# Performance work log

Measured on AMD Instinct MI355X. Metric: run time of the kernel, lower is better.

The kernel has to match this reference:

```python
import jax, jax.numpy as jnp
import numpy as np

N_NODES = 100000
N_EDGES = 1280000
IN_DIM = 64
OUT_DIM = 64


def setup_inputs() -> dict:
    key = jax.random.key(0)
    k1, k2, k3, k4, k5 = jax.random.split(key, 5)
    features = jax.random.normal(k1, (N_NODES, IN_DIM), dtype=jnp.float32)
    w = jax.random.uniform(k2, (N_EDGES,), dtype=jnp.float32)
    # torch nn.Linear weight is [out, in]; we store it as [in, out] so h @ W
    W = jax.random.normal(k3, (IN_DIM, OUT_DIM), dtype=jnp.float32) * (1.0 / np.sqrt(IN_DIM))
    src = jax.random.randint(k4, (N_EDGES,), 0, N_NODES, dtype=jnp.int64 if jax.config.jax_enable_x64 else jnp.int32)
    dst = jax.random.randint(k5, (N_EDGES,), 0, N_NODES, dtype=jnp.int64 if jax.config.jax_enable_x64 else jnp.int32)
    return {"features": features, "w": w, "W": W, "src": src, "dst": dst}


def reference(features, w, W, src, dst):
    num_nodes = features.shape[0]
    # u_mul_e: per-edge message = h[src] * w  (edge-weighted SpMM gather-multiply)
    msg = features[src] * w[:, None]                     # [E, in_dim]
    # fn.sum('m','h'): scatter-add messages to destination nodes
    agg = jax.ops.segment_sum(msg, dst, num_segments=num_nodes)  # [N, in_dim]
    # D_in = 1 / clamp(in_degree, min=1)
    deg = jax.ops.segment_sum(jnp.ones_like(w), dst, num_segments=num_nodes)
    d_in = 1.0 / jnp.maximum(deg, 1.0)                   # [N]
    h = agg * d_in[:, None]
    # linear (bias=False), activation None, batch_norm False, dropout 0
    return h @ W                                         # [N, out_dim]
```

## Files before the change

### kernel.cpp

```cpp
#include <hip/hip_runtime.h>

#define N_NODES 100000
#define N_EDGES 1280000
#define DIM 64
#define NBINS 391
#define CAP 3712
#define EPB 4096
#define NFB 313
#define CONVB 512
#define NTILES 1563
#define FPAD 68
#define WSCALE (1.0f / 32767.0f)

__device__ __forceinline__ unsigned bf16_rne(float x) {
    unsigned u = __float_as_uint(x);
    return (u + 0x7fffu + ((u >> 16) & 1u)) >> 16;
}
__device__ __forceinline__ float bf_lo(unsigned q) { return __uint_as_float(q << 16); }
__device__ __forceinline__ float bf_hi(unsigned q) { return __uint_as_float(q & 0xffff0000u); }

__global__ __launch_bounds__(256) void k_fill_conv(
    const int* __restrict__ src, const float* __restrict__ w,
    const int* __restrict__ dst, int* __restrict__ cursor,
    uint2* __restrict__ binned,
    const float* __restrict__ feat, const float* __restrict__ W,
    unsigned short* __restrict__ fW) {
    __shared__ union U {
        struct { int h[NBINS]; int base_[NBINS]; } fill;
        struct { float w[DIM * DIM]; float f[64 * FPAD]; } conv;
        __device__ U() {}
    } sm;
    int t = threadIdx.x;

    if (blockIdx.x < NFB) {
        for (int i = t; i < NBINS; i += 256) sm.fill.h[i] = 0;
        __syncthreads();
        int eb = blockIdx.x * EPB;
        int d[16], sv[16];
        unsigned wq[16];
        #pragma unroll
        for (int j = 0; j < 16; ++j) {
            int e = eb + j * 256 + t;
            if (e < N_EDGES) {
                d[j] = dst[e];
                sv[j] = src[e];
                wq[j] = (unsigned)(w[e] * 32767.0f + 0.5f);
                atomicAdd(&sm.fill.h[d[j] >> 8], 1);
            } else d[j] = -1;
        }
        __syncthreads();
        for (int i = t; i < NBINS; i += 256) {
            int c = sm.fill.h[i];
            sm.fill.base_[i] = c ? atomicAdd(&cursor[i], c) : 0;
            sm.fill.h[i] = 0;
        }
        __syncthreads();
        #pragma unroll
        for (int j = 0; j < 16; ++j) {
            if (d[j] >= 0) {
                int bin = d[j] >> 8;
                int pos = sm.fill.base_[bin] + atomicAdd(&sm.fill.h[bin], 1);
                binned[bin * CAP + pos] =
                    make_uint2((unsigned)sv[j] | ((unsigned)(d[j] & 255) << 17), wq[j]);
            }
        }
    } else {
        #pragma unroll
        for (int i = 0; i < DIM * DIM / 256; ++i)
            sm.conv.w[t + i * 256] = W[t + i * 256];
        const float4* lds_w4 = (const float4*)sm.conv.w;
        float4* lds_f4 = (float4*)sm.conv.f;
        int tx = t & 15, ny = t >> 4;
        int rr = t >> 2, seg = t & 3;

        for (int tb = blockIdx.x - NFB; tb < NTILES; tb += CONVB) {
            int nb = tb * 64;
            __syncthreads();
            #pragma unroll
            for (int q = 0; q < 4; ++q) {
                float4 v = (nb + rr < N_NODES)
                           ? ((const float4*)feat)[(size_t)(nb + rr) * 16 + seg * 4 + q]
                           : make_float4(0.f, 0.f, 0.f, 0.f);
                lds_f4[(rr * FPAD + seg * 16 + q * 4) >> 2] = v;
            }
            __syncthreads();
            float acc[4][4];
            #pragma unroll
            for (int i = 0; i < 4; ++i)
                #pragma unroll
                for (int j = 0; j < 4; ++j) acc[i][j] = 0.f;
            for (int k0 = 0; k0 < DIM; k0 += 4) {
                float4 hv[4], wv[4];
                #pragma unroll
                for (int i = 0; i < 4; ++i)
                    hv[i] = lds_f4[((ny * 4 + i) * FPAD + k0) >> 2];
                #pragma unroll
                for (int j = 0; j < 4; ++j)
                    wv[j] = lds_w4[((k0 + j) * DIM + tx * 4) >> 2];
                #pragma unroll
                for (int i = 0; i < 4; ++i) {
                    const float* hp = (const float*)&hv[i];
                    #pragma unroll
                    for (int kk = 0; kk < 4; ++kk) {
                        float hk = hp[kk];
                        acc[i][0] = fmaf(hk, ((const float*)&wv[kk])[0], acc[i][0]);
                        acc[i][1] = fmaf(hk, ((const float*)&wv[kk])[1], acc[i][1]);
                        acc[i][2] = fmaf(hk, ((const float*)&wv[kk])[2], acc[i][2]);
                        acc[i][3] = fmaf(hk, ((const float*)&wv[kk])[3], acc[i][3]);
                    }
                }
            }
            #pragma unroll
            for (int i = 0; i < 4; ++i) {
                int node = nb + ny * 4 + i;
                if (node < N_NODES) {
                    ushort4 o;
                    o.x = (unsigned short)bf16_rne(acc[i][0]);
                    o.y = (unsigned short)bf16_rne(acc[i][1]);
                    o.z = (unsigned short)bf16_rne(acc[i][2]);
                    o.w = (unsigned short)bf16_rne(acc[i][3]);
                    *(ushort4*)(fW + (size_t)node * DIM + tx * 4) = o;
                }
            }
        }
    }
}

__global__ __launch_bounds__(256) void k_sortbin(const uint2* __restrict__ binned,
                                                 const int* __restrict__ cursor,
                                                 unsigned* __restrict__ csrp,
                                                 int* __restrict__ offs,
                                                 int* __restrict__ cnt) {
    __shared__ int h[256];
    __shared__ int excl[256];
    __shared__ unsigned stage[CAP];
    int b = blockIdx.x, t = threadIdx.x;
    int total = cursor[b];
    int segbase = b * CAP;
    h[t] = 0;
    __syncthreads();
    for (int i = t; i < total; i += 256)
        atomicAdd(&h[(binned[segbase + i].x >> 17) & 255], 1);
    __syncthreads();
    int v = h[t];
    excl[t] = v;
    __syncthreads();
    for (int off = 1; off < 256; off <<= 1) {
        int add = (t >= off) ? excl[t - off] : 0;
        __syncthreads();
        excl[t] += add;
        __syncthreads();
    }
    int ex = excl[t] - v;
    excl[t] = ex;
    int node = (b << 8) + t;
    if (node < N_NODES) { cnt[node] = v; offs[node] = segbase + ex; }
    h[t] = 0;
    __syncthreads();
    for (int i = t; i < total; i += 256) {
        uint2 e = binned[segbase + i];
        int o = (e.x >> 17) & 255;
        int pos = excl[o] + atomicAdd(&h[o], 1);
        if (pos < CAP) stage[pos] = (e.x & 0x1ffffu) | (e.y << 17);
    }
    __syncthreads();
    for (int i = t; i < total; i += 256)
        csrp[segbase + i] = stage[i];
}

__global__ __launch_bounds__(256) void k_gather(const uint4* __restrict__ fW4,
                                                const unsigned* __restrict__ csrp,
                                                const int* __restrict__ offs,
                                                const int* __restrict__ cnt,
                                                float* __restrict__ out) {
    int lane = threadIdx.x & 63;
    int g = lane >> 3, s = lane & 7;
    int wave = (blockIdx.x * 256 + threadIdx.x) >> 6;
    int nw = gridDim.x * 4;

    for (int node = wave; node < N_NODES; node += nw) {
        int start = offs[node];
        int c = cnt[node];
        int end = start + c;
        float a[8] = {0, 0, 0, 0, 0, 0, 0, 0};
        for (int i = start; i < end; i += 16) {
            int i0 = i + g, i1 = i + 8 + g;
            unsigned p0 = csrp[(i0 < end) ? i0 : start];
            unsigned p1 = csrp[(i1 < end) ? i1 : start];
            float w0 = (i0 < end) ? (float)(p0 >> 17) * WSCALE : 0.f;
            float w1 = (i1 < end) ? (float)(p1 >> 17) * WSCALE : 0.f;
            uint4 q0 = fW4[((p0 & 0x1ffffu) << 3) + s];
            uint4 q1 = fW4[((p1 & 0x1ffffu) << 3) + s];
            a[0] = fmaf(bf_lo(q0.x), w0, a[0]); a[1] = fmaf(bf_hi(q0.x), w0, a[1]);
            a[2] = fmaf(bf_lo(q0.y), w0, a[2]); a[3] = fmaf(bf_hi(q0.y), w0, a[3]);
            a[4] = fmaf(bf_lo(q0.z), w0, a[4]); a[5] = fmaf(bf_hi(q0.z), w0, a[5]);
            a[6] = fmaf(bf_lo(q0.w), w0, a[6]); a[7] = fmaf(bf_hi(q0.w), w0, a[7]);
            a[0] = fmaf(bf_lo(q1.x), w1, a[0]); a[1] = fmaf(bf_hi(q1.x), w1, a[1]);
            a[2] = fmaf(bf_lo(q1.y), w1, a[2]); a[3] = fmaf(bf_hi(q1.y), w1, a[3]);
            a[4] = fmaf(bf_lo(q1.z), w1, a[4]); a[5] = fmaf(bf_hi(q1.z), w1, a[5]);
            a[6] = fmaf(bf_lo(q1.w), w1, a[6]); a[7] = fmaf(bf_hi(q1.w), w1, a[7]);
        }
        #pragma unroll
        for (int j = 0; j < 8; ++j) {
            a[j] += __shfl_xor(a[j], 8, 64);
            a[j] += __shfl_xor(a[j], 16, 64);
            a[j] += __shfl_xor(a[j], 32, 64);
        }
        float dinv = 1.0f / fmaxf((float)c, 1.0f);
        if (g == 0) {
            float4 o0, o1;
            o0.x = a[0] * dinv; o0.y = a[1] * dinv; o0.z = a[2] * dinv; o0.w = a[3] * dinv;
            o1.x = a[4] * dinv; o1.y = a[5] * dinv; o1.z = a[6] * dinv; o1.w = a[7] * dinv;
            ((float4*)out)[node * 16 + s * 2 + 0] = o0;
            ((float4*)out)[node * 16 + s * 2 + 1] = o1;
        }
    }
}

extern "C" void kernel_launch(void* const* d_in, const int* in_sizes, int n_in,
                              void* d_out, int out_size, void* d_ws, size_t ws_size,
                              hipStream_t stream) {
    const float* feat = (const float*)d_in[0];
    const float* w    = (const float*)d_in[1];
    const float* W    = (const float*)d_in[2];
    const int*   src  = (const int*)d_in[3];
    const int*   dst  = (const int*)d_in[4];
    float* out = (float*)d_out;

    unsigned short* fW = (unsigned short*)d_ws;
    uint2* binned  = (uint2*)(fW + (size_t)N_NODES * DIM);
    unsigned* csrp = (unsigned*)(binned + (size_t)NBINS * CAP);
    int* offs      = (int*)(csrp + (size_t)NBINS * CAP);
    int* cnt       = offs + N_NODES;
    int* cursor    = cnt + N_NODES;

    hipMemsetAsync(cursor, 0, NBINS * sizeof(int), stream);

    k_fill_conv<<<NFB + CONVB, 256, 0, stream>>>(src, w, dst, cursor, binned,
                                                 feat, W, fW);
    k_sortbin<<<NBINS, 256, 0, stream>>>(binned, cursor, csrp, offs, cnt);
    k_gather<<<4096, 256, 0, stream>>>((const uint4*)fW, csrp, offs, cnt, out);
}
```

Baseline: 156.1 us.

## Fuse bin sort and gather into one kernel using LDS-resident CSR

Merges the per-bin counting sort and the gather/aggregate kernel into a single 512-thread kernel. The sorted edge list stays in shared memory and the per-node offsets and counts come from the shared histogram and scan, so the csrp/offs/cnt global round trips and one kernel launch are removed. In exchange, the gather now runs on only 391 blocks of 8 waves each instead of 4096 blocks. That lowers the parallelism available to hide the latency of the random feature loads.

```diff
diff --git a/kernel.cpp b/kernel.cpp
--- a/kernel.cpp
+++ b/kernel.cpp
@@ -126,69 +126,55 @@
     }
 }
 
-__global__ __launch_bounds__(256) void k_sortbin(const uint2* __restrict__ binned,
-                                                 const int* __restrict__ cursor,
-                                                 unsigned* __restrict__ csrp,
-                                                 int* __restrict__ offs,
-                                                 int* __restrict__ cnt) {
+__global__ __launch_bounds__(512) void k_sortgather(
+    const uint2* __restrict__ binned, const int* __restrict__ cursor,
+    const uint4* __restrict__ fW4, float* __restrict__ out) {
     __shared__ int h[256];
     __shared__ int excl[256];
     __shared__ unsigned stage[CAP];
     int b = blockIdx.x, t = threadIdx.x;
     int total = cursor[b];
-    int segbase = b * CAP;
-    h[t] = 0;
-    __syncthreads();
-    for (int i = t; i < total; i += 256)
-        atomicAdd(&h[(binned[segbase + i].x >> 17) & 255], 1);
-    __syncthreads();
-    int v = h[t];
-    excl[t] = v;
+    const uint2* seg = binned + b * CAP;
+
+    if (t < 256) h[t] = 0;
+    __syncthreads();
+    for (int i = t; i < total; i += 512)
+        atomicAdd(&h[(seg[i].x >> 17) & 255], 1);
+    __syncthreads();
+    int v = 0;
+    if (t < 256) { v = h[t]; excl[t] = v; }
     __syncthreads();
     for (int off = 1; off < 256; off <<= 1) {
-        int add = (t >= off) ? excl[t - off] : 0;
-        __syncthreads();
-        excl[t] += add;
-        __syncthreads();
-    }
-    int ex = excl[t] - v;
-    excl[t] = ex;
-    int node = (b << 8) + t;
-    if (node < N_NODES) { cnt[node] = v; offs[node] = segbase + ex; }
-    h[t] = 0;
-    __syncthreads();
-    for (int i = t; i < total; i += 256) {
-        uint2 e = binned[segbase + i];
+        int add = 0;
+        if (t < 256 && t >= off) add = excl[t - off];
+        __syncthreads();
+        if (t < 256) excl[t] += add;
+        __syncthreads();
+    }
+    if (t < 256) { excl[t] -= v; h[t] = 0; }
+    __syncthreads();
+    for (int i = t; i < total; i += 512) {
+        uint2 e = seg[i];
         int o = (e.x >> 17) & 255;
         int pos = excl[o] + atomicAdd(&h[o], 1);
         if (pos < CAP) stage[pos] = (e.x & 0x1ffffu) | (e.y << 17);
     }
     __syncthreads();
-    for (int i = t; i < total; i += 256)
-        csrp[segbase + i] = stage[i];
-}
-
-__global__ __launch_bounds__(256) void k_gather(const uint4* __restrict__ fW4,
-                                                const unsigned* __restrict__ csrp,
-                                                const int* __restrict__ offs,
-                                                const int* __restrict__ cnt,
-                                                float* __restrict__ out) {
-    int lane = threadIdx.x & 63;
+    int lane = t & 63, wv = t >> 6;
     int g = lane >> 3, s = lane & 7;
-    int wave = (blockIdx.x * 256 + threadIdx.x) >> 6;
-    int nw = gridDim.x * 4;
-
-    for (int node = wave; node < N_NODES; node += nw) {
-        int start = offs[node];
-        int c = cnt[node];
-        int end = start + c;
+    for (int loc = wv; loc < 256; loc += 8) {
+        int node = (b << 8) + loc;
+        if (node >= N_NODES) break;
+        int st = excl[loc];
+        int c = h[loc];
+        int en = st + c;
         float a[8] = {0, 0, 0, 0, 0, 0, 0, 0};
-        for (int i = start; i < end; i += 16) {
+        for (int i = st; i < en; i += 16) {
             int i0 = i + g, i1 = i + 8 + g;
-            unsigned p0 = csrp[(i0 < end) ? i0 : start];
-            unsigned p1 = csrp[(i1 < end) ? i1 : start];
-            float w0 = (i0 < end) ? (float)(p0 >> 17) * WSCALE : 0.f;
-            float w1 = (i1 < end) ? (float)(p1 >> 17) * WSCALE : 0.f;
+            unsigned p0 = stage[(i0 < en) ? i0 : st];
+            unsigned p1 = stage[(i1 < en) ? i1 : st];
+            float w0 = (i0 < en) ? (float)(p0 >> 17) * WSCALE : 0.f;
+            float w1 = (i1 < en) ? (float)(p1 >> 17) * WSCALE : 0.f;
             uint4 q0 = fW4[((p0 & 0x1ffffu) << 3) + s];
             uint4 q1 = fW4[((p1 & 0x1ffffu) << 3) + s];
             a[0] = fmaf(bf_lo(q0.x), w0, a[0]); a[1] = fmaf(bf_hi(q0.x), w0, a[1]);
@@ -229,15 +215,11 @@
 
     unsigned short* fW = (unsigned short*)d_ws;
     uint2* binned  = (uint2*)(fW + (size_t)N_NODES * DIM);
-    unsigned* csrp = (unsigned*)(binned + (size_t)NBINS * CAP);
-    int* offs      = (int*)(csrp + (size_t)NBINS * CAP);
-    int* cnt       = offs + N_NODES;
-    int* cursor    = cnt + N_NODES;
+    int* cursor    = (int*)(binned + (size_t)NBINS * CAP);
 
     hipMemsetAsync(cursor, 0, NBINS * sizeof(int), stream);
 
     k_fill_conv<<<NFB + CONVB, 256, 0, stream>>>(src, w, dst, cursor, binned,
                                                  feat, W, fW);
-    k_sortbin<<<NBINS, 256, 0, stream>>>(binned, cursor, csrp, offs, cnt);
-    k_gather<<<4096, 256, 0, stream>>>((const uint4*)fW, csrp, offs, cnt, out);
-}
+    k_sortgather<<<NBINS, 512, 0, stream>>>(binned, cursor, (const uint4*)fW, out);
+}
```

Result: slower. 159.8 us (+2.3%).
